# Performance work log

Hardware: AMD Instinct MI355X
Metric: run time of the kernel (lower is better)

Reference implementation:

```python
import jax, jax.numpy as jnp
import numpy as np

D_MODEL = 1024
NUM_HEADS = 16


def setup_inputs() -> dict:
    key = jax.random.key(0)
    ks = jax.random.split(key, 5)
    x = jax.random.normal(ks[0], (1, 4096, D_MODEL), dtype=jnp.float32)
    # Linear stores weight as [out_features, in_features]; init ~ trunc_normal, scaled for stability
    scale = 0.02
    wq = jax.random.normal(ks[1], (D_MODEL, D_MODEL), dtype=jnp.float32) * scale
    wk = jax.random.normal(ks[2], (D_MODEL, D_MODEL), dtype=jnp.float32) * scale
    wv = jax.random.normal(ks[3], (D_MODEL, D_MODEL), dtype=jnp.float32) * scale
    wo = jax.random.normal(ks[4], (D_MODEL, D_MODEL), dtype=jnp.float32) * scale
    return {"x": x, "wq": wq, "wk": wk, "wv": wv, "wo": wo}


def reference(x, wq, wk, wv, wo):
    # x: [B, S, D]; weights: [D, D] stored as [out, in] (y = x @ W.T)
    B, S, D = x.shape
    H = NUM_HEADS
    d_k = D // H
    q = x @ wq.T  # [B, S, D]
    k = x @ wk.T
    v = x @ wv.T
    # torch.split along last dim == reshape into contiguous head chunks
    qh = q.reshape(B, S, H, d_k).transpose(0, 2, 1, 3)  # [B, H, S, d_k]
    kh = k.reshape(B, S, H, d_k).transpose(0, 2, 1, 3)
    vh = v.reshape(B, S, H, d_k).transpose(0, 2, 1, 3)
    scores = jnp.einsum("bhqd,bhkd->bhqk", qh, kh) / jnp.sqrt(jnp.asarray(d_k, x.dtype))
    causal = jnp.tril(jnp.ones((S, S), dtype=bool))
    # original uses masked_fill(mask == 0, -10000.0), not -inf
    scores = jnp.where(causal, scores, jnp.asarray(-10000.0, x.dtype))
    attn = jax.nn.softmax(scores, axis=-1)  # stable (subtracts max), same math as module's Softmax
    ctx = jnp.einsum("bhqk,bhkd->bhqd", attn, vh)  # [B, H, S, d_k]
    ctx = ctx.transpose(0, 2, 1, 3).reshape(B, S, D)  # concat heads along last dim
    return ctx @ wo.T
```

## Files before the change

### kernel.cpp

```cpp
#include <hip/hip_runtime.h>
#include <stdint.h>

typedef short s16x8 __attribute__((ext_vector_type(8)));
typedef float f32x4 __attribute__((ext_vector_type(4)));
typedef float f32x16 __attribute__((ext_vector_type(16)));
typedef unsigned short u16;

#define S_LEN 4096
#define DM    1024
#define NH    16

__device__ __forceinline__ u16 f2bf(float f) {
  unsigned int u; __builtin_memcpy(&u, &f, 4);
  return (u16)((u + 0x7fffu + ((u >> 16) & 1u)) >> 16);
}

__device__ __forceinline__ float exp2_raw(float x) {
  float r;
  asm("v_exp_f32 %0, %1" : "=v"(r) : "v"(x));
  return r;
}

__device__ __forceinline__ void glds16(const void* gsrc, void* lds_uniform) {
  __builtin_amdgcn_global_load_lds(
      (const __attribute__((address_space(1))) unsigned int*)gsrc,
      (__attribute__((address_space(3))) unsigned int*)(unsigned int)(uintptr_t)lds_uniform,
      16, 0, 0);
}

__global__ __launch_bounds__(256)
void cast_all(const float* __restrict__ x,  const float* __restrict__ wq,
              const float* __restrict__ wk, const float* __restrict__ wv,
              const float* __restrict__ wo,
              u16* __restrict__ xb,  u16* __restrict__ wqb, u16* __restrict__ wkb,
              u16* __restrict__ wvb, u16* __restrict__ wob) {
  const int i = blockIdx.x * 256 + threadIdx.x;
  const float* src; u16* dst; int off;
  if (i < (1 << 20)) { src = x; dst = xb; off = i; }
  else {
    const int j = i - (1 << 20);
    const int seg = j >> 18;
    off = j & ((1 << 18) - 1);
    if (seg == 0)      { src = wq; dst = wqb; }
    else if (seg == 1) { src = wk; dst = wkb; }
    else if (seg == 2) { src = wv; dst = wvb; }
    else               { src = wo; dst = wob; }
  }
  float4 v = ((const float4*)src)[off];
  ushort4 o;
  o.x = f2bf(v.x); o.y = f2bf(v.y); o.z = f2bf(v.z); o.w = f2bf(v.w);
  ((ushort4*)dst)[off] = o;
}

#define GEMM_PROLOGUE()                                                        \
  __shared__ u16 SM[32768];                                                    \
  const int tid  = threadIdx.x;                                                \
  const int lane = tid & 63;                                                   \
  const int wave = tid >> 6;                                                   \
  const int g    = lane >> 4;                                                  \
  const int lr   = lane & 15;                                                  \
  const int x7   = lane & 7;                                                   \
  const int wr   = wave >> 1;                                                  \
  const int wc   = wave & 1;                                                   \
  const int a_base = wr * 8192 + lr * 128 + ((g ^ x7) << 4);                   \
  const int b_base = 0x8000 + wc * 8192 + lr * 128 + ((g ^ x7) << 4);          \
  const int stg_row = wave * 8 + (lane >> 3);                                  \
  const int gc      = (lane & 7) ^ (lane >> 3);                                \
  const int stg_dst = wave * 1024;                                             \
  const f32x4 zz = {0.f, 0.f, 0.f, 0.f};                                       \
  f32x4 acc[4][4];                                                             \
  _Pragma("unroll") for (int i = 0; i < 4; ++i)                                \
      _Pragma("unroll") for (int j = 0; j < 4; ++j) acc[i][j] = zz;

#define GEMM_KLOOP(Aptr, Wptr)                                                 \
  const u16* pa0 = Aptr + (size_t)(m0 +  0 + stg_row) * 1024 + gc * 8;         \
  const u16* pa1 = Aptr + (size_t)(m0 + 32 + stg_row) * 1024 + gc * 8;         \
  const u16* pa2 = Aptr + (size_t)(m0 + 64 + stg_row) * 1024 + gc * 8;         \
  const u16* pa3 = Aptr + (size_t)(m0 + 96 + stg_row) * 1024 + gc * 8;         \
  const u16* pw0 = Wptr + (size_t)(n0 +  0 + stg_row) * 1024 + gc * 8;         \
  const u16* pw1 = Wptr + (size_t)(n0 + 32 + stg_row) * 1024 + gc * 8;         \
  const u16* pw2 = Wptr + (size_t)(n0 + 64 + stg_row) * 1024 + gc * 8;         \
  const u16* pw3 = Wptr + (size_t)(n0 + 96 + stg_row) * 1024 + gc * 8;         \
  {                                                                            \
    glds16(pa0, (char*)SM + stg_dst);                                          \
    glds16(pa1, (char*)SM + 4096  + stg_dst);                                  \
    glds16(pa2, (char*)SM + 8192  + stg_dst);                                  \
    glds16(pa3, (char*)SM + 12288 + stg_dst);                                  \
    glds16(pw0, (char*)SM + 0x8000 + stg_dst);                                 \
    glds16(pw1, (char*)SM + 0x8000 + 4096  + stg_dst);                         \
    glds16(pw2, (char*)SM + 0x8000 + 8192  + stg_dst);                         \
    glds16(pw3, (char*)SM + 0x8000 + 12288 + stg_dst);                         \
  }                                                                            \
  int abuf = 0;                                                                \
  for (int kt = 0; kt < 16; ++kt) {                                            \
    if (kt + 1 < 16) {                                                         \
      pa0 += 64; pa1 += 64; pa2 += 64; pa3 += 64;                              \
      pw0 += 64; pw1 += 64; pw2 += 64; pw3 += 64;                              \
      const int nb = abuf ^ 0x4000;                                            \
      glds16(pa0, (char*)SM + nb + stg_dst);                                   \
      glds16(pa1, (char*)SM + nb + 4096  + stg_dst);                           \
      glds16(pa2, (char*)SM + nb + 8192  + stg_dst);                           \
      glds16(pa3, (char*)SM + nb + 12288 + stg_dst);                           \
      glds16(pw0, (char*)SM + 0x8000 + nb + stg_dst);                          \
      glds16(pw1, (char*)SM + 0x8000 + nb + 4096  + stg_dst);                  \
      glds16(pw2, (char*)SM + 0x8000 + nb + 8192  + stg_dst);                  \
      glds16(pw3, (char*)SM + 0x8000 + nb + 12288 + stg_dst);                  \
      asm volatile("s_waitcnt vmcnt(8)" ::: "memory");                         \
    } else {                                                                   \
      asm volatile("s_waitcnt vmcnt(0)" ::: "memory");                         \
    }                                                                          \
    __builtin_amdgcn_sched_barrier(0);                                         \
    __builtin_amdgcn_s_barrier();               \
    __builtin_amdgcn_sched_barrier(0);                                         \
    const int aoff = a_base + abuf;                                            \
    const int boff = b_base + abuf;                                            \
    _Pragma("unroll")                                                          \
    for (int kk = 0; kk < 2; ++kk) {                                           \
      const int ak = aoff ^ (kk << 6);                                         \
      const int bk = boff ^ (kk << 6);                                         \
      s16x8 af[4], bfr[4];                                                     \
      _Pragma("unroll") for (int mi = 0; mi < 4; ++mi)                         \
        af[mi] = *(const s16x8*)((const char*)SM + ak + mi * 2048);            \
      _Pragma("unroll") for (int nj = 0; nj < 4; ++nj)                         \
        bfr[nj] = *(const s16x8*)((const char*)SM + bk + nj * 2048);           \
      _Pragma("unroll") for (int mi = 0; mi < 4; ++mi)                         \
        _Pragma("unroll") for (int nj = 0; nj < 4; ++nj)                       \
          acc[mi][nj] = __builtin_amdgcn_mfma_f32_16x16x32_bf16(               \
              af[mi], bfr[nj], acc[mi][nj], 0, 0, 0);                          \
    }                                                                          \
    asm volatile("s_waitcnt lgkmcnt(0)" ::: "memory");                         \
    __builtin_amdgcn_sched_barrier(0);                                         \
    __builtin_amdgcn_s_barrier();             \
    __builtin_amdgcn_sched_barrier(0);                                         \
    abuf ^= 0x4000;                                                            \
  }

__global__ __launch_bounds__(256)
void gemm_qkv(const u16* __restrict__ A, const u16* __restrict__ Wq,
              const u16* __restrict__ Wk, const u16* __restrict__ Wv,
              u16* __restrict__ Qo, u16* __restrict__ Ko, u16* __restrict__ VTo,
              float qscale) {
  const int m0 = blockIdx.y * 128;
  const int n0 = blockIdx.x * 128;
  const int z  = blockIdx.z;
  const u16* W = (z == 0) ? Wq : ((z == 1) ? Wk : Wv);
  GEMM_PROLOGUE();
  GEMM_KLOOP(A, W);

  const float scale = (z == 0) ? qscale : 1.0f;
  u16* outMK = (z == 0) ? Qo : Ko;
#pragma unroll
  for (int mi = 0; mi < 4; ++mi)
#pragma unroll
    for (int nj = 0; nj < 4; ++nj)
#pragma unroll
      for (int r = 0; r < 4; ++r) {
        const int m = m0 + wr * 64 + mi * 16 + g * 4 + r;
        const int n = n0 + wc * 64 + nj * 16 + lr;
        const u16 v = f2bf(acc[mi][nj][r] * scale);
        if (z < 2) outMK[(size_t)m * 1024 + n] = v;
        else {
          const int mp = (m & ~0x0C) | ((m & 0x04) << 1) | ((m & 0x08) >> 1);
          VTo[(size_t)n * S_LEN + mp] = v;
        }
      }
}

__global__ __launch_bounds__(256)
void gemm_o(const u16* __restrict__ A, const u16* __restrict__ W, float* __restrict__ C) {
  const int m0 = blockIdx.y * 128;
  const int n0 = blockIdx.x * 128;
  GEMM_PROLOGUE();
  GEMM_KLOOP(A, W);

#pragma unroll
  for (int mi = 0; mi < 4; ++mi)
#pragma unroll
    for (int nj = 0; nj < 4; ++nj)
#pragma unroll
      for (int r = 0; r < 4; ++r) {
        const int m = m0 + wr * 64 + mi * 16 + g * 4 + r;
        const int n = n0 + wc * 64 + nj * 16 + lr;
        C[(size_t)m * 1024 + n] = acc[mi][nj][r];
      }
}

__global__ __launch_bounds__(256, 4)
void attn_kernel(const u16* __restrict__ Q, const u16* __restrict__ Kg,
                 const u16* __restrict__ VT, u16* __restrict__ Ctx) {
  __shared__ u16 SM[16384];
  const int tid  = threadIdx.x;
  const int lane = tid & 63;
  const int wave = tid >> 6;
  const int qh   = wave >> 1;
  const int kh   = wave & 1;
  const int l31  = lane & 31;
  const int hi   = lane >> 5;
  const int x7   = lane & 7;
  const int q8   = l31 >> 3;
  const int h  = blockIdx.x;
  const int qi = (int)gridDim.y - 1 - (int)blockIdx.y;
  const int q0 = qi * 64;
  const int qg = q0 + 32 * qh + l31;
  const int nt = qi + 1;

  const int k_base = (32 * kh + l31) * 128;

  const int stg_row = wave * 8 + (lane >> 3);
  const int gcs     = (lane & 7) ^ (lane >> 3) ^ wave;
  const int stg_dst = wave * 1024;
  const u16* kp0 = Kg + (size_t)(stg_row)      * DM + h * 64 + gcs * 8;
  const u16* kp1 = Kg + (size_t)(stg_row + 32) * DM + h * 64 + gcs * 8;
  const u16* vp0 = VT + (size_t)(h * 64 + stg_row)      * S_LEN + gcs * 8;
  const u16* vp1 = VT + (size_t)(h * 64 + stg_row + 32) * S_LEN + gcs * 8;

  s16x8 qf[4];
#pragma unroll
  for (int s = 0; s < 4; ++s)
    qf[s] = *(const s16x8*)(Q + (size_t)qg * DM + h * 64 + 16 * s + 8 * hi);

  f32x16 ctx0 = {0,0,0,0,0,0,0,0,0,0,0,0,0,0,0,0};
  f32x16 ctx1 = ctx0;
  const f32x16 zz16 = ctx0;
  float lsum = 0.f;

  auto STAGE = [&](int t, int ibuf) {
    const size_t koff = (size_t)t * 64 * DM;
    const int   voff  = t * 64;
    const int   kb    = ibuf << 13;
    glds16(kp0 + koff, (char*)SM + kb + stg_dst);
    glds16(kp1 + koff, (char*)SM + kb + 4096 + stg_dst);
    glds16(vp0 + voff, (char*)SM + 0x4000 + kb + stg_dst);
    glds16(vp1 + voff, (char*)SM + 0x4000 + kb + 4096 + stg_dst);
  };

  STAGE(0, 0);
  if (1 < nt) STAGE(1, 1);
  int ib = 0;

  for (int kt = 0; kt < nt; ++kt) {
    const int k0 = kt * 64;
    if (kt + 1 < nt) asm volatile("s_waitcnt vmcnt(4)" ::: "memory");
    else             asm volatile("s_waitcnt vmcnt(0)" ::: "memory");
    __builtin_amdgcn_sched_barrier(0);
    __builtin_amdgcn_s_barrier();
    __builtin_amdgcn_sched_barrier(0);

    const int kb = ib << 13;
    const int kbase_abs = k0 + 32 * kh;
    const bool active = (kbase_abs <= q0 + 32 * qh + 31);
    if (active) {
      f32x16 st = zz16;
      __builtin_amdgcn_s_setprio(1);
#pragma unroll
      for (int s = 0; s < 4; ++s) {
        s16x8 kf = *(const s16x8*)((const char*)SM + kb + k_base +
                                   ((((2 * s + hi) ^ x7) ^ q8) << 4));
        st = __builtin_amdgcn_mfma_f32_32x32x16_bf16(kf, qf[s], st, 0, 0, 0);
      }
      __builtin_amdgcn_s_setprio(0);

      float ex[16];
      const bool anyMask = (kbase_abs + 31 > q0 + 32 * qh);
      if (anyMask) {
#pragma unroll
        for (int r = 0; r < 16; ++r) {
          const int kpos = kbase_abs + (r & 3) + 8 * (r >> 2) + 4 * hi;
          float e = exp2_raw(st[r]);
          ex[r] = (kpos > qg) ? 0.f : e;
        }
      } else {
#pragma unroll
        for (int r = 0; r < 16; ++r) ex[r] = exp2_raw(st[r]);
      }
      float s4[4];
#pragma unroll
      for (int i = 0; i < 4; ++i)
        s4[i] = (ex[4 * i] + ex[4 * i + 1]) + (ex[4 * i + 2] + ex[4 * i + 3]);
      lsum += (s4[0] + s4[1]) + (s4[2] + s4[3]);

      union Pu { s16x8 v; unsigned int u[4]; } P[2];
#pragma unroll
      for (int s = 0; s < 2; ++s)
#pragma unroll
        for (int w = 0; w < 4; ++w)
          asm("v_cvt_pk_bf16_f32 %0, %1, %2"
              : "=v"(P[s].u[w])
              : "v"(ex[s * 8 + 2 * w]), "v"(ex[s * 8 + 2 * w + 1]));

      __builtin_amdgcn_s_setprio(1);
#pragma unroll
      for (int s = 0; s < 2; ++s) {
        const int ch = (((4 * kh + 2 * s + hi) ^ x7) ^ q8) << 4;
        s16x8 v0 = *(const s16x8*)((const char*)SM + 0x4000 + kb + l31 * 128 + ch);
        ctx0 = __builtin_amdgcn_mfma_f32_32x32x16_bf16(v0, P[s].v, ctx0, 0, 0, 0);
        s16x8 v1 = *(const s16x8*)((const char*)SM + 0x4000 + kb + (32 + l31) * 128 + ch);
        ctx1 = __builtin_amdgcn_mfma_f32_32x32x16_bf16(v1, P[s].v, ctx1, 0, 0, 0);
      }
      __builtin_amdgcn_s_setprio(0);
    }

    asm volatile("s_waitcnt lgkmcnt(0)" ::: "memory");
    __builtin_amdgcn_sched_barrier(0);
    __builtin_amdgcn_s_barrier();
    __builtin_amdgcn_sched_barrier(0);
    if (kt + 2 < nt) STAGE(kt + 2, ib);
    ib ^= 1;
  }

  lsum += __shfl_xor(lsum, 32);
  const int pbase = qh * 0x2800;
  if (kh == 1) {
#pragma unroll
    for (int r = 0; r < 16; ++r) {
      const int drow = (r & 3) + 8 * (r >> 2) + 4 * hi;
      *(float*)((char*)SM + pbase + ((drow)      * 32 + l31) * 4) = ctx0[r];
      *(float*)((char*)SM + pbase + ((32 + drow) * 32 + l31) * 4) = ctx1[r];
    }
    if (lane < 32) *(float*)((char*)SM + pbase + 0x2000 + l31 * 4) = lsum;
  }
  __syncthreads();
  if (kh == 0) {
    const float ls1 = *(const float*)((const char*)SM + pbase + 0x2000 + l31 * 4);
    const float inv = 1.0f / (lsum + ls1);
    u16* outp = Ctx + (size_t)qg * DM + h * 64;
#pragma unroll
    for (int r = 0; r < 16; ++r) {
      const int drow = (r & 3) + 8 * (r >> 2) + 4 * hi;
      const float c0 = ctx0[r] + *(const float*)((const char*)SM + pbase + ((drow) * 32 + l31) * 4);
      const float c1 = ctx1[r] + *(const float*)((const char*)SM + pbase + ((32 + drow) * 32 + l31) * 4);
      outp[drow]      = f2bf(c0 * inv);
      outp[32 + drow] = f2bf(c1 * inv);
    }
  }
}

extern "C" void kernel_launch(void* const* d_in, const int* in_sizes, int n_in,
                              void* d_out, int out_size, void* d_ws, size_t ws_size,
                              hipStream_t stream) {
  const float* x  = (const float*)d_in[0];
  const float* wq = (const float*)d_in[1];
  const float* wk = (const float*)d_in[2];
  const float* wv = (const float*)d_in[3];
  const float* wo = (const float*)d_in[4];

  u16* p = (u16*)d_ws;
  u16* xb  = p; p += (size_t)S_LEN * DM;
  u16* wqb = p; p += (size_t)DM * DM;
  u16* wkb = p; p += (size_t)DM * DM;
  u16* wvb = p; p += (size_t)DM * DM;
  u16* wob = p; p += (size_t)DM * DM;
  u16* Qb  = p; p += (size_t)S_LEN * DM;
  u16* Kb  = p; p += (size_t)S_LEN * DM;
  u16* VTb = p; p += (size_t)S_LEN * DM;
  u16* Cb  = p; p += (size_t)S_LEN * DM;
  if (ws_size < (size_t)(5 * S_LEN * DM + 4 * DM * DM) * 2) return;

  cast_all<<<dim3((2 * 1024 * 1024) / 256), 256, 0, stream>>>(
      x, wq, wk, wv, wo, xb, wqb, wkb, wvb, wob);

  const float QSCALE = 0.125f * 1.44269504088896f;
  gemm_qkv<<<dim3(DM / 128, S_LEN / 128, 3), 256, 0, stream>>>(
      xb, wqb, wkb, wvb, Qb, Kb, VTb, QSCALE);

  attn_kernel<<<dim3(NH, S_LEN / 64), 256, 0, stream>>>(Qb, Kb, VTb, Cb);

  gemm_o<<<dim3(DM / 128, S_LEN / 128), 256, 0, stream>>>(Cb, wob, (float*)d_out);
}
```

Before: 124.0 us.

## Restructure attention block to two waves each handling both query halves

The attention kernel moves from four waves (two query halves by two key halves) to two waves, each covering one key half for both 32-row query groups. Each K and V fragment read from LDS now feeds two MFMA chains, halving LDS fragment reads per MFMA. Staging issues eight global-to-LDS loads per thread instead of four. The cost is higher register pressure from four context accumulators, and fewer waves per block to hide latency.

```diff
diff --git a/kernel.cpp b/kernel.cpp
--- a/kernel.cpp
+++ b/kernel.cpp
@@ -185,15 +185,13 @@
       }
 }
 
-__global__ __launch_bounds__(256, 4)
+__global__ __launch_bounds__(128, 2)
 void attn_kernel(const u16* __restrict__ Q, const u16* __restrict__ Kg,
                  const u16* __restrict__ VT, u16* __restrict__ Ctx) {
   __shared__ u16 SM[16384];
   const int tid  = threadIdx.x;
   const int lane = tid & 63;
-  const int wave = tid >> 6;
-  const int qh   = wave >> 1;
-  const int kh   = wave & 1;
+  const int kh   = tid >> 6;
   const int l31  = lane & 31;
   const int hi   = lane >> 5;
   const int x7   = lane & 7;
@@ -201,37 +199,48 @@
   const int h  = blockIdx.x;
   const int qi = (int)gridDim.y - 1 - (int)blockIdx.y;
   const int q0 = qi * 64;
-  const int qg = q0 + 32 * qh + l31;
   const int nt = qi + 1;
 
   const int k_base = (32 * kh + l31) * 128;
 
-  const int stg_row = wave * 8 + (lane >> 3);
-  const int gcs     = (lane & 7) ^ (lane >> 3) ^ wave;
-  const int stg_dst = wave * 1024;
-  const u16* kp0 = Kg + (size_t)(stg_row)      * DM + h * 64 + gcs * 8;
-  const u16* kp1 = Kg + (size_t)(stg_row + 32) * DM + h * 64 + gcs * 8;
-  const u16* vp0 = VT + (size_t)(h * 64 + stg_row)      * S_LEN + gcs * 8;
-  const u16* vp1 = VT + (size_t)(h * 64 + stg_row + 32) * S_LEN + gcs * 8;
-
-  s16x8 qf[4];
-#pragma unroll
-  for (int s = 0; s < 4; ++s)
-    qf[s] = *(const s16x8*)(Q + (size_t)qg * DM + h * 64 + 16 * s + 8 * hi);
-
-  f32x16 ctx0 = {0,0,0,0,0,0,0,0,0,0,0,0,0,0,0,0};
-  f32x16 ctx1 = ctx0;
-  const f32x16 zz16 = ctx0;
-  float lsum = 0.f;
+  const int r8  = lane >> 3;
+  const int gcsE = x7 ^ r8 ^ kh;
+  const int gcsO = gcsE ^ 2;
+  const int srow = 8 * kh + r8;
+  const u16* kpt0 = Kg + (size_t)(srow +  0) * DM + h * 64 + gcsE * 8;
+  const u16* kpt1 = Kg + (size_t)(srow + 16) * DM + h * 64 + gcsO * 8;
+  const u16* kpt2 = Kg + (size_t)(srow + 32) * DM + h * 64 + gcsE * 8;
+  const u16* kpt3 = Kg + (size_t)(srow + 48) * DM + h * 64 + gcsO * 8;
+  const u16* vpt0 = VT + (size_t)(h * 64 + srow +  0) * S_LEN + gcsE * 8;
+  const u16* vpt1 = VT + (size_t)(h * 64 + srow + 16) * S_LEN + gcsO * 8;
+  const u16* vpt2 = VT + (size_t)(h * 64 + srow + 32) * S_LEN + gcsE * 8;
+  const u16* vpt3 = VT + (size_t)(h * 64 + srow + 48) * S_LEN + gcsO * 8;
+  const int sd = kh * 1024;
+
+  s16x8 qf0[4], qf1[4];
+#pragma unroll
+  for (int s = 0; s < 4; ++s) {
+    qf0[s] = *(const s16x8*)(Q + (size_t)(q0 + l31) * DM + h * 64 + 16 * s + 8 * hi);
+    qf1[s] = *(const s16x8*)(Q + (size_t)(q0 + 32 + l31) * DM + h * 64 + 16 * s + 8 * hi);
+  }
+
+  f32x16 ctx00 = {0,0,0,0,0,0,0,0,0,0,0,0,0,0,0,0};
+  f32x16 ctx01 = ctx00, ctx10 = ctx00, ctx11 = ctx00;
+  const f32x16 zz16 = ctx00;
+  float lsum0 = 0.f, lsum1 = 0.f;
 
   auto STAGE = [&](int t, int ibuf) {
     const size_t koff = (size_t)t * 64 * DM;
     const int   voff  = t * 64;
     const int   kb    = ibuf << 13;
-    glds16(kp0 + koff, (char*)SM + kb + stg_dst);
-    glds16(kp1 + koff, (char*)SM + kb + 4096 + stg_dst);
-    glds16(vp0 + voff, (char*)SM + 0x4000 + kb + stg_dst);
-    glds16(vp1 + voff, (char*)SM + 0x4000 + kb + 4096 + stg_dst);
+    glds16(kpt0 + koff, (char*)SM + kb + 0    + sd);
+    glds16(kpt1 + koff, (char*)SM + kb + 2048 + sd);
+    glds16(kpt2 + koff, (char*)SM + kb + 4096 + sd);
+    glds16(kpt3 + koff, (char*)SM + kb + 6144 + sd);
+    glds16(vpt0 + voff, (char*)SM + 0x4000 + kb + 0    + sd);
+    glds16(vpt1 + voff, (char*)SM + 0x4000 + kb + 2048 + sd);
+    glds16(vpt2 + voff, (char*)SM + 0x4000 + kb + 4096 + sd);
+    glds16(vpt3 + voff, (char*)SM + 0x4000 + kb + 6144 + sd);
   };
 
   STAGE(0, 0);
@@ -240,7 +249,7 @@
 
   for (int kt = 0; kt < nt; ++kt) {
     const int k0 = kt * 64;
-    if (kt + 1 < nt) asm volatile("s_waitcnt vmcnt(4)" ::: "memory");
+    if (kt + 1 < nt) asm volatile("s_waitcnt vmcnt(8)" ::: "memory");
     else             asm volatile("s_waitcnt vmcnt(0)" ::: "memory");
     __builtin_amdgcn_sched_barrier(0);
     __builtin_amdgcn_s_barrier();
@@ -248,54 +257,91 @@
 
     const int kb = ib << 13;
     const int kbase_abs = k0 + 32 * kh;
-    const bool active = (kbase_abs <= q0 + 32 * qh + 31);
-    if (active) {
-      f32x16 st = zz16;
+    const bool act0 = (kbase_abs <= q0 + 31);
+    {
+      f32x16 st0 = zz16, st1 = zz16;
       __builtin_amdgcn_s_setprio(1);
 #pragma unroll
       for (int s = 0; s < 4; ++s) {
         s16x8 kf = *(const s16x8*)((const char*)SM + kb + k_base +
                                    ((((2 * s + hi) ^ x7) ^ q8) << 4));
-        st = __builtin_amdgcn_mfma_f32_32x32x16_bf16(kf, qf[s], st, 0, 0, 0);
+        if (act0) st0 = __builtin_amdgcn_mfma_f32_32x32x16_bf16(kf, qf0[s], st0, 0, 0, 0);
+        st1 = __builtin_amdgcn_mfma_f32_32x32x16_bf16(kf, qf1[s], st1, 0, 0, 0);
       }
       __builtin_amdgcn_s_setprio(0);
 
-      float ex[16];
-      const bool anyMask = (kbase_abs + 31 > q0 + 32 * qh);
-      if (anyMask) {
-#pragma unroll
-        for (int r = 0; r < 16; ++r) {
-          const int kpos = kbase_abs + (r & 3) + 8 * (r >> 2) + 4 * hi;
-          float e = exp2_raw(st[r]);
-          ex[r] = (kpos > qg) ? 0.f : e;
+      union Pu { s16x8 v; unsigned int u[4]; } P0[2], P1[2];
+      if (act0) {
+        float ex[16];
+        const bool anyMask = (kbase_abs + 31 > q0);
+        if (anyMask) {
+#pragma unroll
+          for (int r = 0; r < 16; ++r) {
+            const int kpos = kbase_abs + (r & 3) + 8 * (r >> 2) + 4 * hi;
+            float e = exp2_raw(st0[r]);
+            ex[r] = (kpos > q0 + l31) ? 0.f : e;
+          }
+        } else {
+#pragma unroll
+          for (int r = 0; r < 16; ++r) ex[r] = exp2_raw(st0[r]);
         }
-      } else {
-#pragma unroll
-        for (int r = 0; r < 16; ++r) ex[r] = exp2_raw(st[r]);
-      }
-      float s4[4];
-#pragma unroll
-      for (int i = 0; i < 4; ++i)
-        s4[i] = (ex[4 * i] + ex[4 * i + 1]) + (ex[4 * i + 2] + ex[4 * i + 3]);
-      lsum += (s4[0] + s4[1]) + (s4[2] + s4[3]);
-
-      union Pu { s16x8 v; unsigned int u[4]; } P[2];
-#pragma unroll
-      for (int s = 0; s < 2; ++s)
-#pragma unroll
-        for (int w = 0; w < 4; ++w)
-          asm("v_cvt_pk_bf16_f32 %0, %1, %2"
-              : "=v"(P[s].u[w])
-              : "v"(ex[s * 8 + 2 * w]), "v"(ex[s * 8 + 2 * w + 1]));
+        float s4[4];
+#pragma unroll
+        for (int i = 0; i < 4; ++i)
+          s4[i] = (ex[4 * i] + ex[4 * i + 1]) + (ex[4 * i + 2] + ex[4 * i + 3]);
+        lsum0 += (s4[0] + s4[1]) + (s4[2] + s4[3]);
+#pragma unroll
+        for (int s = 0; s < 2; ++s)
+#pragma unroll
+          for (int w = 0; w < 4; ++w)
+            asm("v_cvt_pk_bf16_f32 %0, %1, %2"
+                : "=v"(P0[s].u[w])
+                : "v"(ex[s * 8 + 2 * w]), "v"(ex[s * 8 + 2 * w + 1]));
+      }
+      {
+        float ex[16];
+        const bool anyMask = (kbase_abs + 31 > q0 + 32);
+        if (anyMask) {
+#pragma unroll
+          for (int r = 0; r < 16; ++r) {
+            const int kpos = kbase_abs + (r & 3) + 8 * (r >> 2) + 4 * hi;
+            float e = exp2_raw(st1[r]);
+            ex[r] = (kpos > q0 + 32 + l31) ? 0.f : e;
+          }
+        } else {
+#pragma unroll
+          for (int r = 0; r < 16; ++r) ex[r] = exp2_raw(st1[r]);
+        }
+        float s4[4];
+#pragma unroll
+        for (int i = 0; i < 4; ++i)
+          s4[i] = (ex[4 * i] + ex[4 * i + 1]) + (ex[4 * i + 2] + ex[4 * i + 3]);
+        lsum1 += (s4[0] + s4[1]) + (s4[2] + s4[3]);
+#pragma unroll
+        for (int s = 0; s < 2; ++s)
+#pragma unroll
+          for (int w = 0; w < 4; ++w)
+            asm("v_cvt_pk_bf16_f32 %0, %1, %2"
+                : "=v"(P1[s].u[w])
+                : "v"(ex[s * 8 + 2 * w]), "v"(ex[s * 8 + 2 * w + 1]));
+      }
 
       __builtin_amdgcn_s_setprio(1);
 #pragma unroll
       for (int s = 0; s < 2; ++s) {
         const int ch = (((4 * kh + 2 * s + hi) ^ x7) ^ q8) << 4;
         s16x8 v0 = *(const s16x8*)((const char*)SM + 0x4000 + kb + l31 * 128 + ch);
-        ctx0 = __builtin_amdgcn_mfma_f32_32x32x16_bf16(v0, P[s].v, ctx0, 0, 0, 0);
         s16x8 v1 = *(const s16x8*)((const char*)SM + 0x4000 + kb + (32 + l31) * 128 + ch);
-        ctx1 = __builtin_amdgcn_mfma_f32_32x32x16_bf16(v1, P[s].v, ctx1, 0, 0, 0);
+        if (act0) {
+          if (s == 0) { ctx00 = __builtin_amdgcn_mfma_f32_32x32x16_bf16(v0, P0[0].v, ctx00, 0, 0, 0);
+                        ctx01 = __builtin_amdgcn_mfma_f32_32x32x16_bf16(v1, P0[0].v, ctx01, 0, 0, 0); }
+          else        { ctx00 = __builtin_amdgcn_mfma_f32_32x32x16_bf16(v0, P0[1].v, ctx00, 0, 0, 0);
+                        ctx01 = __builtin_amdgcn_mfma_f32_32x32x16_bf16(v1, P0[1].v, ctx01, 0, 0, 0); }
+        }
+        if (s == 0) { ctx10 = __builtin_amdgcn_mfma_f32_32x32x16_bf16(v0, P1[0].v, ctx10, 0, 0, 0);
+                      ctx11 = __builtin_amdgcn_mfma_f32_32x32x16_bf16(v1, P1[0].v, ctx11, 0, 0, 0); }
+        else        { ctx10 = __builtin_amdgcn_mfma_f32_32x32x16_bf16(v0, P1[1].v, ctx10, 0, 0, 0);
+                      ctx11 = __builtin_amdgcn_mfma_f32_32x32x16_bf16(v1, P1[1].v, ctx11, 0, 0, 0); }
       }
       __builtin_amdgcn_s_setprio(0);
     }
@@ -308,29 +354,35 @@
     ib ^= 1;
   }
 
-  lsum += __shfl_xor(lsum, 32);
-  const int pbase = qh * 0x2800;
+  lsum0 += __shfl_xor(lsum0, 32);
+  lsum1 += __shfl_xor(lsum1, 32);
   if (kh == 1) {
 #pragma unroll
     for (int r = 0; r < 16; ++r) {
       const int drow = (r & 3) + 8 * (r >> 2) + 4 * hi;
-      *(float*)((char*)SM + pbase + ((drow)      * 32 + l31) * 4) = ctx0[r];
-      *(float*)((char*)SM + pbase + ((32 + drow) * 32 + l31) * 4) = ctx1[r];
+      *(float*)((char*)SM + (drow)        * 128 + l31 * 4) = ctx00[r];
+      *(float*)((char*)SM + (32 + drow)   * 128 + l31 * 4) = ctx01[r];
+      *(float*)((char*)SM + 8192 + (drow)      * 128 + l31 * 4) = ctx10[r];
+      *(float*)((char*)SM + 8192 + (32 + drow) * 128 + l31 * 4) = ctx11[r];
     }
-    if (lane < 32) *(float*)((char*)SM + pbase + 0x2000 + l31 * 4) = lsum;
+    if (lane < 32) {
+      *(float*)((char*)SM + 16384 + l31 * 4)       = lsum0;
+      *(float*)((char*)SM + 16384 + 128 + l31 * 4) = lsum1;
+    }
   }
   __syncthreads();
   if (kh == 0) {
-    const float ls1 = *(const float*)((const char*)SM + pbase + 0x2000 + l31 * 4);
-    const float inv = 1.0f / (lsum + ls1);
-    u16* outp = Ctx + (size_t)qg * DM + h * 64;
+    const float inv0 = 1.0f / (lsum0 + *(const float*)((const char*)SM + 16384 + l31 * 4));
+    const float inv1 = 1.0f / (lsum1 + *(const float*)((const char*)SM + 16384 + 128 + l31 * 4));
+    u16* out0 = Ctx + (size_t)(q0 + l31) * DM + h * 64;
+    u16* out1 = Ctx + (size_t)(q0 + 32 + l31) * DM + h * 64;
 #pragma unroll
     for (int r = 0; r < 16; ++r) {
       const int drow = (r & 3) + 8 * (r >> 2) + 4 * hi;
-      const float c0 = ctx0[r] + *(const float*)((const char*)SM + pbase + ((drow) * 32 + l31) * 4);
-      const float c1 = ctx1[r] + *(const float*)((const char*)SM + pbase + ((32 + drow) * 32 + l31) * 4);
-      outp[drow]      = f2bf(c0 * inv);
-      outp[32 + drow] = f2bf(c1 * inv);
+      out0[drow]      = f2bf((ctx00[r] + *(const float*)((const char*)SM + (drow) * 128 + l31 * 4)) * inv0);
+      out0[32 + drow] = f2bf((ctx01[r] + *(const float*)((const char*)SM + (32 + drow) * 128 + l31 * 4)) * inv0);
+      out1[drow]      = f2bf((ctx10[r] + *(const float*)((const char*)SM + 8192 + (drow) * 128 + l31 * 4)) * inv1);
+      out1[32 + drow] = f2bf((ctx11[r] + *(const float*)((const char*)SM + 8192 + (32 + drow) * 128 + l31 * 4)) * inv1);
     }
   }
 }
@@ -363,7 +415,7 @@
   gemm_qkv<<<dim3(DM / 128, S_LEN / 128, 3), 256, 0, stream>>>(
       xb, wqb, wkb, wvb, Qb, Kb, VTb, QSCALE);
 
-  attn_kernel<<<dim3(NH, S_LEN / 64), 256, 0, stream>>>(Qb, Kb, VTb, Cb);
+  attn_kernel<<<dim3(NH, S_LEN / 64), 128, 0, stream>>>(Qb, Kb, VTb, Cb);
 
   gemm_o<<<dim3(DM / 128, S_LEN / 128), 256, 0, stream>>>(Cb, wob, (float*)d_out);
 }
```

Result: slower. 140.1 us (+13.0%).
